# Kernel optimization log

Hardware: AMD Instinct MI355X
Metric: run time of the kernel (lower is better)

## Reference

```python
import jax, jax.numpy as jnp
import numpy as np

K = 10  # knn_graph default neighbors (self excluded)
NEG = 0.2  # LeakyReLU slope


def lrelu(x):
    return jnp.where(x > 0, x, NEG * x)


def conv1x1_1d(x, w):  # x: (B,Ci,N), w: (Co,Ci)
    return jnp.einsum('oi,bin->bon', w, x)


def conv1x1_2d(x, w):  # x: (B,Ci,N,k), w: (Co,Ci)
    return jnp.einsum('oi,bink->bonk', w, x)


def bn1(x, s, b):  # folded eval-mode BN, x: (B,C,N)
    return x * s[None, :, None] + b[None, :, None]


def bn2(x, s, b):  # x: (B,C,N,k)
    return x * s[None, :, None, None] + b[None, :, None, None]


def knn_graph(x, k=K):
    # x: (B, D, N) -> edge features (B, 2D, N, k)
    xt = jnp.transpose(x, (0, 2, 1))  # (B,N,D)
    sq = jnp.sum(xt * xt, axis=-1)  # (B,N)
    d2 = sq[:, :, None] + sq[:, None, :] - 2.0 * jnp.einsum('bnd,bmd->bnm', xt, xt)
    _, idx = jax.lax.top_k(-d2, k + 1)  # nearest k+1 incl. self
    idx = idx[:, :, 1:]  # drop self -> (B,N,k)
    B = xt.shape[0]
    feats = xt[jnp.arange(B)[:, None, None], idx]  # (B,N,k,D)
    center = xt[:, :, None, :]  # (B,N,1,D)
    edge = jnp.concatenate((feats - center, jnp.broadcast_to(center, feats.shape)), axis=-1)
    return jnp.transpose(edge, (0, 3, 1, 2))  # (B,2D,N,k)


def _make_params(key):
    ks = iter(jax.random.split(key, 32))
    def W(co, ci):
        return jax.random.normal(next(ks), (co, ci), jnp.float32) * (1.0 / np.sqrt(ci))
    def SB(c):
        return (jax.random.uniform(next(ks), (c,), jnp.float32, 0.5, 1.5),
                jax.random.normal(next(ks), (c,), jnp.float32) * 0.1)
    p = {}
    p['w1'] = W(64, 6);    p['s1'], p['b1'] = SB(64)
    p['w2'] = W(64, 64);   p['s2'], p['b2'] = SB(64)
    p['w3'] = W(64, 128);  p['s3'], p['b3'] = SB(64)
    p['w4'] = W(64, 64);   p['s4'], p['b4'] = SB(64)
    p['w5'] = W(64, 128);  p['s5'], p['b5'] = SB(64)
    p['w6'] = W(1024, 192); p['s6'], p['b6'] = SB(1024)
    p['w7'] = W(64, 16);   p['s7'], p['b7'] = SB(64)
    p['wp1'] = W(256, 1280); p['sp1'], p['bp1'] = SB(256)
    p['wp2'] = W(256, 256);  p['sp2'], p['bp2'] = SB(256)
    p['wp3'] = W(128, 256);  p['sp3'], p['bp3'] = SB(128)
    p['wp4'] = W(6, 128)
    return p


def setup_inputs() -> dict:
    key = jax.random.key(0)
    k0, k1, k2 = jax.random.split(key, 3)
    inp = {
        'points': jax.random.normal(k0, (8, 2048, 3), jnp.float32),
        'label': jax.random.uniform(k1, (8, 16), jnp.float32),
    }
    inp.update(_make_params(k2))
    return inp


def reference(points, label,
              w1, s1, b1, w2, s2, b2, w3, s3, b3, w4, s4, b4, w5, s5, b5,
              w6, s6, b6, w7, s7, b7,
              wp1, sp1, bp1, wp2, sp2, bp2, wp3, sp3, bp3, wp4):
    B, N, _ = points.shape
    x0 = jnp.transpose(points, (0, 2, 1))  # (B,3,N)

    e1 = knn_graph(x0)                                   # (B,6,N,k)
    h = lrelu(bn2(conv1x1_2d(e1, w1), s1, b1))
    out1 = jnp.max(lrelu(bn2(conv1x1_2d(h, w2), s2, b2)), axis=-1)  # (B,64,N)

    e2 = knn_graph(out1)                                 # (B,128,N,k)
    h = lrelu(bn2(conv1x1_2d(e2, w3), s3, b3))
    out2 = jnp.max(lrelu(bn2(conv1x1_2d(h, w4), s4, b4)), axis=-1)  # (B,64,N)

    e3 = knn_graph(out2)                                 # (B,128,N,k)
    out3 = jnp.max(lrelu(bn2(conv1x1_2d(e3, w5), s5, b5)), axis=-1)  # (B,64,N)

    comb = jnp.concatenate((out1, out2, out3), axis=1)   # (B,192,N)
    out4 = lrelu(bn1(conv1x1_1d(comb, w6), s6, b6))      # (B,1024,N)
    out4 = jnp.max(out4, axis=-1, keepdims=True)         # (B,1024,1)

    cat_vet = lrelu(bn1(conv1x1_1d(label[:, :, None], w7), s7, b7))  # (B,64,1)
    glob = jnp.broadcast_to(jnp.concatenate((out4, cat_vet), axis=1), (B, 1088, N))

    out = jnp.concatenate((out1, out2, out3, glob), axis=1)  # (B,1280,N)
    out = lrelu(bn1(conv1x1_1d(out, wp1), sp1, bp1))
    out = lrelu(bn1(conv1x1_1d(out, wp2), sp2, bp2))  # dropout = identity (eval)
    out = lrelu(bn1(conv1x1_1d(out, wp3), sp3, bp3))
    out = conv1x1_1d(out, wp4)                         # (B,6,N)
    return jnp.transpose(out, (0, 2, 1))               # (B,N,6)
```

## Files before the change

kernel.cpp:

```cpp
#include <hip/hip_runtime.h>
#include <float.h>

#define NEG 0.2f
constexpr int BATCH = 8;
constexpr int NPTS  = 2048;
constexpr int KNN   = 10;
constexpr int KP1   = 11;

__device__ __forceinline__ float lrelu(float x) { return x > 0.f ? x : NEG * x; }

__device__ __forceinline__ unsigned long long dkey(float d, int m) {
    unsigned u = __float_as_uint(d);
    u ^= (unsigned)((int)u >> 31) | 0x80000000u;
    return ((unsigned long long)u << 32) | (unsigned)m;
}

template<int D>
__global__ void sq_kernel(const float* __restrict__ xt, float* __restrict__ sq) {
    int i = blockIdx.x * 256 + threadIdx.x;
    if (i >= BATCH * NPTS) return;
    const float* p = xt + (size_t)i * D;
    float s = 0.f;
    #pragma unroll
    for (int d = 0; d < D; ++d) s += p[d] * p[d];
    sq[i] = s;
}

__global__ void sq64_kernel(const float* __restrict__ xt, float* __restrict__ sq) {
    int i = blockIdx.x * 256 + threadIdx.x;
    if (i >= BATCH * NPTS) return;
    const float4* p = (const float4*)(xt + (size_t)i * 64);
    float4 s4 = {0.f, 0.f, 0.f, 0.f};
    #pragma unroll
    for (int d = 0; d < 16; ++d) {
        float4 v = p[d];
        s4.x += v.x * v.x; s4.y += v.y * v.y; s4.z += v.z * v.z; s4.w += v.w * v.w;
    }
    sq[i] = (s4.x + s4.y) + (s4.z + s4.w);
}

__global__ __launch_bounds__(64) void knn3_kernel(const float* __restrict__ xt,
                                                  const float* __restrict__ sq,
                                                  int* __restrict__ idx_out) {
    const int bn = blockIdx.x;
    const int b  = bn >> 11;
    const int l  = threadIdx.x;

    const float qx = xt[(size_t)bn * 3 + 0];
    const float qy = xt[(size_t)bn * 3 + 1];
    const float qz = xt[(size_t)bn * 3 + 2];
    const float sqn = sq[bn];
    const float* xb  = xt + (size_t)b * NPTS * 3;
    const float* sqb_ = sq + (size_t)b * NPTS;

    unsigned long long lk[KP1];
    #pragma unroll
    for (int j = 0; j < KP1; ++j) lk[j] = ~0ULL;

    for (int m = l; m < NPTS; m += 64) {
        float dot = 0.f;
        dot += qx * xb[m * 3 + 0];
        dot += qy * xb[m * 3 + 1];
        dot += qz * xb[m * 3 + 2];
        float cd = sqn + sqb_[m] - 2.f * dot;
        unsigned long long key = dkey(cd, m);
        if (key < lk[KP1 - 1]) {
            #pragma unroll
            for (int j = 0; j < KP1; ++j) {
                bool better = key < lk[j];
                unsigned long long tk = lk[j];
                if (better) { lk[j] = key; key = tk; }
            }
        }
    }

    #pragma unroll
    for (int k = 0; k < KP1; ++k) {
        unsigned long long mk = lk[0];
        #pragma unroll
        for (int s = 32; s >= 1; s >>= 1) {
            unsigned long long o = __shfl_xor(mk, s, 64);
            mk = (o < mk) ? o : mk;
        }
        if (k >= 1 && l == k - 1)
            idx_out[(size_t)bn * KNN + (k - 1)] = (int)(unsigned)mk;
        if (lk[0] == mk) {
            #pragma unroll
            for (int j = 0; j < KP1 - 1; ++j) lk[j] = lk[j + 1];
            lk[KP1 - 1] = ~0ULL;
        }
    }
}

__global__ __launch_bounds__(256) void knn64_kernel(const float* __restrict__ xt,
                                                    const float* __restrict__ sq,
                                                    int* __restrict__ idx_out) {
    const int t  = threadIdx.x;
    const int qg = t >> 5;
    const int lc = t & 31;
    const int h  = qg & 1;
    const int w  = t >> 6;
    const int bn0 = blockIdx.x * 8;
    const int bn  = bn0 + qg;
    const int qA  = bn0 + 2 * w;
    const int qB  = qA + 1;
    const int b   = bn >> 11;
    const float* xb = xt + (size_t)b * NPTS * 64;

    __shared__ __align__(16) float4 tile4[2][32][16];

    float4 xqa[8], xqb[8];
    {
        const float4* pa = (const float4*)(xt + (size_t)qA * 64 + h * 32);
        const float4* pb = (const float4*)(xt + (size_t)qB * 64 + h * 32);
        #pragma unroll
        for (int i = 0; i < 8; ++i) { xqa[i] = pa[i]; xqb[i] = pb[i]; }
    }
    const float sqn = sq[bn];
    const float* sqb_ = sq + b * NPTS;

    unsigned long long lk[KP1];
    #pragma unroll
    for (int j = 0; j < KP1; ++j) lk[j] = ~0ULL;

    const int ci  = t >> 3;
    const int sub = t & 7;

    int ro[8];
    #pragma unroll
    for (int i = 0; i < 8; ++i) ro[i] = (h * 8 + i) ^ (lc & 15);
    const int wo0 = (2 * sub)     ^ (ci & 15);
    const int wo1 = (2 * sub + 1) ^ (ci & 15);

    const float4* rb0 = &tile4[0][lc][0];
    const float4* rb1 = &tile4[1][lc][0];
    float4*       wb0 = &tile4[0][ci][0];
    float4*       wb1 = &tile4[1][ci][0];

    const float4* src = (const float4*)(xb + (size_t)ci * 64 + sub * 8);

    {
        float4 u0 = src[0], u1 = src[1];
        wb0[wo0] = u0;
        wb0[wo1] = u1;
    }
    __syncthreads();
    src += 512;

    for (int t0 = 0; t0 < NPTS; t0 += 32) {
        float4 n0, n1;
        const bool more = (t0 + 32 < NPTS);
        if (more) { n0 = src[0]; n1 = src[1]; }

        float a0 = 0.f, a1 = 0.f, a2 = 0.f, a3 = 0.f;
        float c0 = 0.f, c1 = 0.f, c2 = 0.f, c3 = 0.f;
        #pragma unroll
        for (int i = 0; i < 8; ++i) {
            float4 v = rb0[ro[i]];
            a0 += xqa[i].x * v.x; a1 += xqa[i].y * v.y;
            a2 += xqa[i].z * v.z; a3 += xqa[i].w * v.w;
            c0 += xqb[i].x * v.x; c1 += xqb[i].y * v.y;
            c2 += xqb[i].z * v.z; c3 += xqb[i].w * v.w;
        }
        float pA = (a0 + a1) + (a2 + a3);
        float pB = (c0 + c1) + (c2 + c3);
        float oA = __shfl_xor(pA, 32, 64);
        float oB = __shfl_xor(pB, 32, 64);
        float dot = (h == 0) ? (pA + oA) : (oB + pB);

        const int m = t0 + lc;
        float cd = sqn + sqb_[m] - 2.f * dot;
        unsigned long long key = dkey(cd, m);
        if (key < lk[KP1 - 1]) {
            #pragma unroll
            for (int j = 0; j < KP1; ++j) {
                bool better = key < lk[j];
                unsigned long long tk = lk[j];
                if (better) { lk[j] = key; key = tk; }
            }
        }

        if (more) {
            wb1[wo0] = n0;
            wb1[wo1] = n1;
        }
        __syncthreads();
        { const float4* tr = rb0; rb0 = rb1; rb1 = tr; }
        { float4* tw = wb0; wb0 = wb1; wb1 = tw; }
        src += 512;
    }

    #pragma unroll
    for (int k = 0; k < KP1; ++k) {
        unsigned long long mk = lk[0];
        #pragma unroll
        for (int s = 16; s >= 1; s >>= 1) {
            unsigned long long o = __shfl_xor(mk, s, 32);
            mk = (o < mk) ? o : mk;
        }
        if (k >= 1 && lc == k - 1)
            idx_out[(size_t)bn * KNN + (k - 1)] = (int)(unsigned)mk;
        if (lk[0] == mk) {
            #pragma unroll
            for (int j = 0; j < KP1 - 1; ++j) lk[j] = lk[j + 1];
            lk[KP1 - 1] = ~0ULL;
        }
    }
}

__global__ __launch_bounds__(256) void edgeconv1_kernel(
    const float* __restrict__ pts, const int* __restrict__ idx,
    const float* __restrict__ w1, const float* __restrict__ s1, const float* __restrict__ b1,
    const float* __restrict__ w2, const float* __restrict__ s2, const float* __restrict__ b2,
    float* __restrict__ outt) {
    const int p0g = blockIdx.x * 8;
    const int b   = p0g >> 11;
    const int t   = threadIdx.x;
    const int p   = t >> 5;
    const int c32 = t & 31;
    const int pn  = p0g + p;
    const int c0 = c32, c1 = c32 + 32;

    __shared__ int   sidx[8][KNN];
    __shared__ float h1s[8][KNN][64];

    if (t < 8 * KNN) sidx[t / KNN][t % KNN] = idx[(size_t)(p0g + t / KNN) * KNN + (t % KNN)];
    __syncthreads();

    const float cx = pts[pn * 3 + 0], cy = pts[pn * 3 + 1], cz = pts[pn * 3 + 2];
    float w1r0[6], w1r1[6];
    #pragma unroll
    for (int i = 0; i < 6; ++i) { w1r0[i] = w1[c0 * 6 + i]; w1r1[i] = w1[c1 * 6 + i]; }
    const float s1c0 = s1[c0], b1c0 = b1[c0], s1c1 = s1[c1], b1c1 = b1[c1];

    #pragma unroll
    for (int k = 0; k < KNN; ++k) {
        const int m = sidx[p][k];
        const float* f = pts + ((size_t)b * NPTS + m) * 3;
        const float e0 = f[0] - cx, e1 = f[1] - cy, e2 = f[2] - cz;
        float a0 = w1r0[0] * e0 + w1r0[1] * e1 + w1r0[2] * e2
                 + w1r0[3] * cx + w1r0[4] * cy + w1r0[5] * cz;
        float a1 = w1r1[0] * e0 + w1r1[1] * e1 + w1r1[2] * e2
                 + w1r1[3] * cx + w1r1[4] * cy + w1r1[5] * cz;
        h1s[p][k][c0] = lrelu(a0 * s1c0 + b1c0);
        h1s[p][k][c1] = lrelu(a1 * s1c1 + b1c1);
    }
    __syncthreads();

    float a20[KNN], a21[KNN];
    #pragma unroll
    for (int k = 0; k < KNN; ++k) { a20[k] = 0.f; a21[k] = 0.f; }
    for (int j4 = 0; j4 < 16; ++j4) {
        float4 wv0 = *(const float4*)&w2[c0 * 64 + j4 * 4];
        float4 wv1 = *(const float4*)&w2[c1 * 64 + j4 * 4];
        #pragma unroll
        for (int k = 0; k < KNN; ++k) {
            float4 h4 = *(const float4*)&h1s[p][k][j4 * 4];
            a20[k] += wv0.x * h4.x + wv0.y * h4.y + wv0.z * h4.z + wv0.w * h4.w;
            a21[k] += wv1.x * h4.x + wv1.y * h4.y + wv1.z * h4.z + wv1.w * h4.w;
        }
    }
    const float s2c0 = s2[c0], b2c0 = b2[c0], s2c1 = s2[c1], b2c1 = b2[c1];
    float mx0 = -FLT_MAX, mx1 = -FLT_MAX;
    #pragma unroll
    for (int k = 0; k < KNN; ++k) {
        mx0 = fmaxf(mx0, lrelu(a20[k] * s2c0 + b2c0));
        mx1 = fmaxf(mx1, lrelu(a21[k] * s2c1 + b2c1));
    }
    outt[(size_t)pn * 64 + c0] = mx0;
    outt[(size_t)pn * 64 + c1] = mx1;
}

__global__ __launch_bounds__(256) void edgeconv2_kernel(
    const float* __restrict__ xin, const int* __restrict__ idx,
    const float* __restrict__ w3, const float* __restrict__ s3, const float* __restrict__ b3,
    const float* __restrict__ w4, const float* __restrict__ s4, const float* __restrict__ b4,
    float* __restrict__ outt) {
    const int p0g = blockIdx.x * 8;
    const int b   = p0g >> 11;
    const int t   = threadIdx.x;
    const int p   = t >> 5;
    const int c32 = t & 31;
    const int pn  = p0g + p;
    const int c0 = c32, c1 = c32 + 32;

    __shared__ int   sidx[8][KNN];
    __shared__ float cens[8][64];
    __shared__ float feas[8][KNN][64];
    __shared__ float h1s[8][KNN][64];

    if (t < 8 * KNN) sidx[t / KNN][t % KNN] = idx[(size_t)(p0g + t / KNN) * KNN + (t % KNN)];
    for (int i = t; i < 8 * 64; i += 256)
        cens[i >> 6][i & 63] = xin[((size_t)p0g + (i >> 6)) * 64 + (i & 63)];
    __syncthreads();
    for (int i = t; i < 8 * KNN * 64; i += 256) {
        int pp = i / (KNN * 64), r = i - pp * (KNN * 64);
        int k = r >> 6, c = r & 63;
        feas[pp][k][c] = xin[((size_t)b * NPTS + sidx[pp][k]) * 64 + c];
    }
    __syncthreads();

    float a0[KNN], a1[KNN];
    #pragma unroll
    for (int k = 0; k < KNN; ++k) { a0[k] = 0.f; a1[k] = 0.f; }
    float4 ab0 = {0.f, 0.f, 0.f, 0.f};
    float4 ab1 = {0.f, 0.f, 0.f, 0.f};
    for (int j4 = 0; j4 < 16; ++j4) {
        float4 wa0 = *(const float4*)&w3[c0 * 128 + j4 * 4];
        float4 wb0 = *(const float4*)&w3[c0 * 128 + 64 + j4 * 4];
        float4 wa1 = *(const float4*)&w3[c1 * 128 + j4 * 4];
        float4 wb1 = *(const float4*)&w3[c1 * 128 + 64 + j4 * 4];
        float4 c4 = *(const float4*)&cens[p][j4 * 4];
        ab0.x += (wb0.x - wa0.x) * c4.x; ab0.y += (wb0.y - wa0.y) * c4.y;
        ab0.z += (wb0.z - wa0.z) * c4.z; ab0.w += (wb0.w - wa0.w) * c4.w;
        ab1.x += (wb1.x - wa1.x) * c4.x; ab1.y += (wb1.y - wa1.y) * c4.y;
        ab1.z += (wb1.z - wa1.z) * c4.z; ab1.w += (wb1.w - wa1.w) * c4.w;
        #pragma unroll
        for (int k = 0; k < KNN; ++k) {
            float4 f4 = *(const float4*)&feas[p][k][j4 * 4];
            a0[k] += wa0.x * f4.x + wa0.y * f4.y + wa0.z * f4.z + wa0.w * f4.w;
            a1[k] += wa1.x * f4.x + wa1.y * f4.y + wa1.z * f4.z + wa1.w * f4.w;
        }
    }
    const float abase0 = (ab0.x + ab0.y) + (ab0.z + ab0.w);
    const float abase1 = (ab1.x + ab1.y) + (ab1.z + ab1.w);
    const float s3c0 = s3[c0], b3c0 = b3[c0], s3c1 = s3[c1], b3c1 = b3[c1];
    #pragma unroll
    for (int k = 0; k < KNN; ++k) {
        h1s[p][k][c0] = lrelu((a0[k] + abase0) * s3c0 + b3c0);
        h1s[p][k][c1] = lrelu((a1[k] + abase1) * s3c1 + b3c1);
    }
    __syncthreads();

    float a20[KNN], a21[KNN];
    #pragma unroll
    for (int k = 0; k < KNN; ++k) { a20[k] = 0.f; a21[k] = 0.f; }
    for (int j4 = 0; j4 < 16; ++j4) {
        float4 wv0 = *(const float4*)&w4[c0 * 64 + j4 * 4];
        float4 wv1 = *(const float4*)&w4[c1 * 64 + j4 * 4];
        #pragma unroll
        for (int k = 0; k < KNN; ++k) {
            float4 h4 = *(const float4*)&h1s[p][k][j4 * 4];
            a20[k] += wv0.x * h4.x + wv0.y * h4.y + wv0.z * h4.z + wv0.w * h4.w;
            a21[k] += wv1.x * h4.x + wv1.y * h4.y + wv1.z * h4.z + wv1.w * h4.w;
        }
    }
    const float s4c0 = s4[c0], b4c0 = b4[c0], s4c1 = s4[c1], b4c1 = b4[c1];
    float mx0 = -FLT_MAX, mx1 = -FLT_MAX;
    #pragma unroll
    for (int k = 0; k < KNN; ++k) {
        mx0 = fmaxf(mx0, lrelu(a20[k] * s4c0 + b4c0));
        mx1 = fmaxf(mx1, lrelu(a21[k] * s4c1 + b4c1));
    }
    outt[(size_t)pn * 64 + c0] = mx0;
    outt[(size_t)pn * 64 + c1] = mx1;
}

__global__ __launch_bounds__(256) void edgeconv3_kernel(
    const float* __restrict__ xin, const int* __restrict__ idx,
    const float* __restrict__ w5, const float* __restrict__ s5, const float* __restrict__ b5,
    float* __restrict__ outt) {
    const int p0g = blockIdx.x * 8;
    const int b   = p0g >> 11;
    const int t   = threadIdx.x;
    const int p   = t >> 5;
    const int c32 = t & 31;
    const int pn  = p0g + p;
    const int c0 = c32, c1 = c32 + 32;

    __shared__ int   sidx[8][KNN];
    __shared__ float cens[8][64];
    __shared__ float feas[8][KNN][64];

    if (t < 8 * KNN) sidx[t / KNN][t % KNN] = idx[(size_t)(p0g + t / KNN) * KNN + (t % KNN)];
    for (int i = t; i < 8 * 64; i += 256)
        cens[i >> 6][i & 63] = xin[((size_t)p0g + (i >> 6)) * 64 + (i & 63)];
    __syncthreads();
    for (int i = t; i < 8 * KNN * 64; i += 256) {
        int pp = i / (KNN * 64), r = i - pp * (KNN * 64);
        int k = r >> 6, c = r & 63;
        feas[pp][k][c] = xin[((size_t)b * NPTS + sidx[pp][k]) * 64 + c];
    }
    __syncthreads();

    float a0[KNN], a1[KNN];
    #pragma unroll
    for (int k = 0; k < KNN; ++k) { a0[k] = 0.f; a1[k] = 0.f; }
    float4 ab0 = {0.f, 0.f, 0.f, 0.f};
    float4 ab1 = {0.f, 0.f, 0.f, 0.f};
    for (int j4 = 0; j4 < 16; ++j4) {
        float4 wa0 = *(const float4*)&w5[c0 * 128 + j4 * 4];
        float4 wb0 = *(const float4*)&w5[c0 * 128 + 64 + j4 * 4];
        float4 wa1 = *(const float4*)&w5[c1 * 128 + j4 * 4];
        float4 wb1 = *(const float4*)&w5[c1 * 128 + 64 + j4 * 4];
        float4 c4 = *(const float4*)&cens[p][j4 * 4];
        ab0.x += (wb0.x - wa0.x) * c4.x; ab0.y += (wb0.y - wa0.y) * c4.y;
        ab0.z += (wb0.z - wa0.z) * c4.z; ab0.w += (wb0.w - wa0.w) * c4.w;
        ab1.x += (wb1.x - wa1.x) * c4.x; ab1.y += (wb1.y - wa1.y) * c4.y;
        ab1.z += (wb1.z - wa1.z) * c4.z; ab1.w += (wb1.w - wa1.w) * c4.w;
        #pragma unroll
        for (int k = 0; k < KNN; ++k) {
            float4 f4 = *(const float4*)&feas[p][k][j4 * 4];
            a0[k] += wa0.x * f4.x + wa0.y * f4.y + wa0.z * f4.z + wa0.w * f4.w;
            a1[k] += wa1.x * f4.x + wa1.y * f4.y + wa1.z * f4.z + wa1.w * f4.w;
        }
    }
    const float abase0 = (ab0.x + ab0.y) + (ab0.z + ab0.w);
    const float abase1 = (ab1.x + ab1.y) + (ab1.z + ab1.w);
    const float s5c0 = s5[c0], b5c0 = b5[c0], s5c1 = s5[c1], b5c1 = b5[c1];
    float mx0 = -FLT_MAX, mx1 = -FLT_MAX;
    #pragma unroll
    for (int k = 0; k < KNN; ++k) {
        mx0 = fmaxf(mx0, lrelu((a0[k] + abase0) * s5c0 + b5c0));
        mx1 = fmaxf(mx1, lrelu((a1[k] + abase1) * s5c1 + b5c1));
    }
    outt[(size_t)pn * 64 + c0] = mx0;
    outt[(size_t)pn * 64 + c1] = mx1;
}

__global__ __launch_bounds__(64) void catvet_kernel(
    const float* __restrict__ label,
    const float* __restrict__ w7, const float* __restrict__ s7, const float* __restrict__ b7,
    float* __restrict__ catv) {
    const int b = blockIdx.x, c = threadIdx.x;
    float a = 0.f;
    #pragma unroll
    for (int i = 0; i < 16; ++i) a += w7[c * 16 + i] * label[b * 16 + i];
    catv[b * 64 + c] = lrelu(a * s7[c] + b7[c]);
}

__global__ void w6t_kernel(const float* __restrict__ w6, float* __restrict__ w6t) {
    int i = blockIdx.x * 256 + threadIdx.x;
    if (i >= 192 * 1024) return;
    int k = i >> 10, c = i & 1023;
    w6t[i] = w6[c * 192 + k];
}

constexpr int OPTS = 32;
__global__ __launch_bounds__(256) void out4max_kernel(
    const float* __restrict__ out1t, const float* __restrict__ out2t, const float* __restrict__ out3t,
    const float* __restrict__ w6t, float* __restrict__ partial) {
    const int blk = blockIdx.x;
    const int b   = blk >> 6;
    const int nt  = blk & 63;
    const int t   = threadIdx.x;

    __shared__ float xs[192 * OPTS];
    for (int idx = t; idx < 192 * OPTS; idx += 256) {
        int p = idx / 192, r = idx - p * 192;
        const size_t gp = (size_t)b * NPTS + nt * OPTS + p;
        float val;
        if (r < 64)       val = out1t[gp * 64 + r];
        else if (r < 128) val = out2t[gp * 64 + (r - 64)];
        else              val = out3t[gp * 64 + (r - 128)];
        xs[r * OPTS + p] = val;
    }
    __syncthreads();

    float mx0 = -FLT_MAX, mx1 = -FLT_MAX, mx2 = -FLT_MAX, mx3 = -FLT_MAX;
    #pragma unroll
    for (int pg = 0; pg < OPTS / 16; ++pg) {
        float acc0[16], acc1[16], acc2[16], acc3[16];
        #pragma unroll
        for (int p = 0; p < 16; ++p) { acc0[p] = 0.f; acc1[p] = 0.f; acc2[p] = 0.f; acc3[p] = 0.f; }
        #pragma unroll 2
        for (int k = 0; k < 192; ++k) {
            float4 wv = *(const float4*)&w6t[(size_t)k * 1024 + t * 4];
            const float4* xr4 = (const float4*)&xs[k * OPTS + pg * 16];
            #pragma unroll
            for (int p4 = 0; p4 < 4; ++p4) {
                float4 xv = xr4[p4];
                acc0[p4 * 4 + 0] += wv.x * xv.x; acc0[p4 * 4 + 1] += wv.x * xv.y;
                acc0[p4 * 4 + 2] += wv.x * xv.z; acc0[p4 * 4 + 3] += wv.x * xv.w;
                acc1[p4 * 4 + 0] += wv.y * xv.x; acc1[p4 * 4 + 1] += wv.y * xv.y;
                acc1[p4 * 4 + 2] += wv.y * xv.z; acc1[p4 * 4 + 3] += wv.y * xv.w;
                acc2[p4 * 4 + 0] += wv.z * xv.x; acc2[p4 * 4 + 1] += wv.z * xv.y;
                acc2[p4 * 4 + 2] += wv.z * xv.z; acc2[p4 * 4 + 3] += wv.z * xv.w;
                acc3[p4 * 4 + 0] += wv.w * xv.x; acc3[p4 * 4 + 1] += wv.w * xv.y;
                acc3[p4 * 4 + 2] += wv.w * xv.z; acc3[p4 * 4 + 3] += wv.w * xv.w;
            }
        }
        #pragma unroll
        for (int p = 0; p < 16; ++p) {
            mx0 = fmaxf(mx0, acc0[p]); mx1 = fmaxf(mx1, acc1[p]);
            mx2 = fmaxf(mx2, acc2[p]); mx3 = fmaxf(mx3, acc3[p]);
        }
    }
    float4 o = {mx0, mx1, mx2, mx3};
    *(float4*)&partial[(size_t)blk * 1024 + t * 4] = o;
}

__global__ __launch_bounds__(256) void out4reduce_kernel(
    const float* __restrict__ partial,
    const float* __restrict__ s6, const float* __restrict__ b6,
    float* __restrict__ out4m) {
    const int i = blockIdx.x * 256 + threadIdx.x;
    const int b = i >> 10, c = i & 1023;
    float m = -FLT_MAX;
    for (int nt = 0; nt < 64; ++nt)
        m = fmaxf(m, partial[((size_t)b * 64 + nt) * 1024 + c]);
    out4m[i] = lrelu(m * s6[c] + b6[c]);
}

__global__ __launch_bounds__(256) void gbias_kernel(
    const float* __restrict__ out4m, const float* __restrict__ catv,
    const float* __restrict__ wp1, float* __restrict__ g) {
    const int b = blockIdx.x, t = threadIdx.x;
    __shared__ float v[1088];
    for (int i = t; i < 1088; i += 256)
        v[i] = (i < 1024) ? out4m[(size_t)b * 1024 + i] : catv[(size_t)b * 64 + (i - 1024)];
    __syncthreads();
    const float* w = wp1 + (size_t)t * 1280 + 192;
    float4 s4 = {0.f, 0.f, 0.f, 0.f};
    for (int i = 0; i < 272; ++i) {
        float4 wv = *(const float4*)&w[i * 4];
        float4 vv = *(const float4*)&v[i * 4];
        s4.x += wv.x * vv.x; s4.y += wv.y * vv.y; s4.z += wv.z * vv.z; s4.w += wv.w * vv.w;
    }
    g[(size_t)b * 256 + t] = (s4.x + s4.y) + (s4.z + s4.w);
}

constexpr int HP = 16;
constexpr int KC = 16;

__global__ __launch_bounds__(256) void head_kernel(
    const float* __restrict__ out1t, const float* __restrict__ out2t, const float* __restrict__ out3t,
    const float* __restrict__ g,
    const float* __restrict__ wp1, const float* __restrict__ sp1, const float* __restrict__ bp1,
    const float* __restrict__ wp2, const float* __restrict__ sp2, const float* __restrict__ bp2,
    const float* __restrict__ wp3, const float* __restrict__ sp3, const float* __restrict__ bp3,
    const float* __restrict__ wp4, float* __restrict__ out) {
    const int p0 = blockIdx.x * HP;
    const int b  = p0 >> 11;
    const int t  = threadIdx.x;

    __shared__ float smA[4096];
    __shared__ float smB[4096];
    __shared__ float smW[KC * 256];

    for (int e = t; e < 192 * HP; e += 256) {
        int p = e / 192, k = e - p * 192;
        float val;
        if (k < 64)       val = out1t[((size_t)(p0 + p)) * 64 + k];
        else if (k < 128) val = out2t[((size_t)(p0 + p)) * 64 + (k - 64)];
        else              val = out3t[((size_t)(p0 + p)) * 64 + (k - 128)];
        smA[k * HP + p] = val;
    }

    const int og = t & 31;
    const int pg = t >> 5;

    float acc[2][8];
    #pragma unroll
    for (int i = 0; i < 8; ++i) {
        float gv = g[(size_t)b * 256 + og * 8 + i];
        acc[0][i] = gv; acc[1][i] = gv;
    }
    for (int kc = 0; kc < 192 / KC; ++kc) {
        __syncthreads();
        #pragma unroll
        for (int it = 0; it < KC; ++it)
            smW[it * 256 + t] = wp1[(size_t)t * 1280 + kc * KC + it];
        __syncthreads();
        #pragma unroll 4
        for (int kk = 0; kk < KC; ++kk) {
            int k = kc * KC + kk;
            float2 xv = *(const float2*)&smA[k * HP + pg * 2];
            float4 w0 = *(const float4*)&smW[kk * 256 + og * 8];
            float4 w1v = *(const float4*)&smW[kk * 256 + og * 8 + 4];
            float wv[8] = {w0.x, w0.y, w0.z, w0.w, w1v.x, w1v.y, w1v.z, w1v.w};
            #pragma unroll
            for (int i = 0; i < 8; ++i) {
                acc[0][i] += xv.x * wv[i];
                acc[1][i] += xv.y * wv[i];
            }
        }
    }
    #pragma unroll
    for (int i = 0; i < 8; ++i) {
        int o = og * 8 + i;
        float sc = sp1[o], bc = bp1[o];
        smB[o * HP + pg * 2 + 0] = lrelu(acc[0][i] * sc + bc);
        smB[o * HP + pg * 2 + 1] = lrelu(acc[1][i] * sc + bc);
    }

    float acc2[2][8];
    #pragma unroll
    for (int i = 0; i < 8; ++i) { acc2[0][i] = 0.f; acc2[1][i] = 0.f; }
    for (int kc = 0; kc < 256 / KC; ++kc) {
        __syncthreads();
        #pragma unroll
        for (int it = 0; it < KC; ++it)
            smW[it * 256 + t] = wp2[(size_t)t * 256 + kc * KC + it];
        __syncthreads();
        #pragma unroll 4
        for (int kk = 0; kk < KC; ++kk) {
            int k = kc * KC + kk;
            float2 xv = *(const float2*)&smB[k * HP + pg * 2];
            float4 w0 = *(const float4*)&smW[kk * 256 + og * 8];
            float4 w1v = *(const float4*)&smW[kk * 256 + og * 8 + 4];
            float wv[8] = {w0.x, w0.y, w0.z, w0.w, w1v.x, w1v.y, w1v.z, w1v.w};
            #pragma unroll
            for (int i = 0; i < 8; ++i) {
                acc2[0][i] += xv.x * wv[i];
                acc2[1][i] += xv.y * wv[i];
            }
        }
    }
    __syncthreads();
    #pragma unroll
    for (int i = 0; i < 8; ++i) {
        int o = og * 8 + i;
        float sc = sp2[o], bc = bp2[o];
        smA[o * HP + pg * 2 + 0] = lrelu(acc2[0][i] * sc + bc);
        smA[o * HP + pg * 2 + 1] = lrelu(acc2[1][i] * sc + bc);
    }

    const int og3 = t & 15;
    const int p3  = t >> 4;
    float acc3[8];
    #pragma unroll
    for (int i = 0; i < 8; ++i) acc3[i] = 0.f;
    for (int kc = 0; kc < 256 / KC; ++kc) {
        __syncthreads();
        for (int e = t; e < KC * 128; e += 256) {
            int kk = e >> 7, o = e & 127;
            smW[kk * 128 + o] = wp3[(size_t)o * 256 + kc * KC + kk];
        }
        __syncthreads();
        #pragma unroll 4
        for (int kk = 0; kk < KC; ++kk) {
            int k = kc * KC + kk;
            float xv = smA[k * HP + p3];
            float4 w0 = *(const float4*)&smW[kk * 128 + og3 * 8];
            float4 w1v = *(const float4*)&smW[kk * 128 + og3 * 8 + 4];
            float wv[8] = {w0.x, w0.y, w0.z, w0.w, w1v.x, w1v.y, w1v.z, w1v.w};
            #pragma unroll
            for (int i = 0; i < 8; ++i) acc3[i] += xv * wv[i];
        }
    }
    __syncthreads();
    #pragma unroll
    for (int i = 0; i < 8; ++i) {
        int o = og3 * 8 + i;
        float sc = sp3[o], bc = bp3[o];
        smB[o * HP + p3] = lrelu(acc3[i] * sc + bc);
    }
    __syncthreads();

    if (t < HP * 6) {
        int p = t / 6, o = t - p * 6;
        float4 s4 = {0.f, 0.f, 0.f, 0.f};
        for (int k4 = 0; k4 < 32; ++k4) {
            float4 wv = *(const float4*)&wp4[o * 128 + k4 * 4];
            s4.x += wv.x * smB[(k4 * 4 + 0) * HP + p];
            s4.y += wv.y * smB[(k4 * 4 + 1) * HP + p];
            s4.z += wv.z * smB[(k4 * 4 + 2) * HP + p];
            s4.w += wv.w * smB[(k4 * 4 + 3) * HP + p];
        }
        out[((size_t)(p0 + p)) * 6 + o] = (s4.x + s4.y) + (s4.z + s4.w);
    }
}

extern "C" void kernel_launch(void* const* d_in, const int* in_sizes, int n_in,
                              void* d_out, int out_size, void* d_ws, size_t ws_size,
                              hipStream_t stream) {
    const float* points = (const float*)d_in[0];
    const float* label  = (const float*)d_in[1];
    const float* w1  = (const float*)d_in[2];
    const float* s1  = (const float*)d_in[3];
    const float* b1  = (const float*)d_in[4];
    const float* w2  = (const float*)d_in[5];
    const float* s2  = (const float*)d_in[6];
    const float* b2  = (const float*)d_in[7];
    const float* w3  = (const float*)d_in[8];
    const float* s3  = (const float*)d_in[9];
    const float* b3  = (const float*)d_in[10];
    const float* w4  = (const float*)d_in[11];
    const float* s4  = (const float*)d_in[12];
    const float* b4  = (const float*)d_in[13];
    const float* w5  = (const float*)d_in[14];
    const float* s5  = (const float*)d_in[15];
    const float* b5  = (const float*)d_in[16];
    const float* w6  = (const float*)d_in[17];
    const float* s6  = (const float*)d_in[18];
    const float* b6  = (const float*)d_in[19];
    const float* w7  = (const float*)d_in[20];
    const float* s7  = (const float*)d_in[21];
    const float* b7  = (const float*)d_in[22];
    const float* wp1 = (const float*)d_in[23];
    const float* sp1 = (const float*)d_in[24];
    const float* bp1 = (const float*)d_in[25];
    const float* wp2 = (const float*)d_in[26];
    const float* sp2 = (const float*)d_in[27];
    const float* bp2 = (const float*)d_in[28];
    const float* wp3 = (const float*)d_in[29];
    const float* sp3 = (const float*)d_in[30];
    const float* bp3 = (const float*)d_in[31];
    const float* wp4 = (const float*)d_in[32];

    float* ws = (float*)d_ws;
    size_t off = 0;
    auto alloc = [&](size_t nf) { float* p = ws + off; off += nf; return p; };
    float* out1t = alloc((size_t)BATCH * NPTS * 64);
    float* out2t = alloc((size_t)BATCH * NPTS * 64);
    float* out3t = alloc((size_t)BATCH * NPTS * 64);
    float* sqb   = alloc((size_t)BATCH * NPTS);
    float* out4m = alloc((size_t)BATCH * 1024);
    float* catv  = alloc((size_t)BATCH * 64);
    float* gb    = alloc((size_t)BATCH * 256);
    float* w6t   = alloc((size_t)192 * 1024);
    float* part  = alloc((size_t)512 * 1024);
    int* idx1 = (int*)alloc((size_t)BATCH * NPTS * KNN);
    int* idx2 = (int*)alloc((size_t)BATCH * NPTS * KNN);
    int* idx3 = (int*)alloc((size_t)BATCH * NPTS * KNN);

    const int BN = BATCH * NPTS;
    const int sqBlocks = (BN + 255) / 256;

    sq_kernel<3><<<sqBlocks, 256, 0, stream>>>(points, sqb);
    knn3_kernel<<<BN, 64, 0, stream>>>(points, sqb, idx1);
    edgeconv1_kernel<<<BN / 8, 256, 0, stream>>>(points, idx1, w1, s1, b1, w2, s2, b2, out1t);

    sq64_kernel<<<sqBlocks, 256, 0, stream>>>(out1t, sqb);
    knn64_kernel<<<BN / 8, 256, 0, stream>>>(out1t, sqb, idx2);
    edgeconv2_kernel<<<BN / 8, 256, 0, stream>>>(out1t, idx2, w3, s3, b3, w4, s4, b4, out2t);

    sq64_kernel<<<sqBlocks, 256, 0, stream>>>(out2t, sqb);
    knn64_kernel<<<BN / 8, 256, 0, stream>>>(out2t, sqb, idx3);
    edgeconv3_kernel<<<BN / 8, 256, 0, stream>>>(out2t, idx3, w5, s5, b5, out3t);

    catvet_kernel<<<BATCH, 64, 0, stream>>>(label, w7, s7, b7, catv);
    w6t_kernel<<<(192 * 1024 + 255) / 256, 256, 0, stream>>>(w6, w6t);
    out4max_kernel<<<512, 256, 0, stream>>>(out1t, out2t, out3t, w6t, part);
    out4reduce_kernel<<<BATCH * 1024 / 256, 256, 0, stream>>>(part, s6, b6, out4m);
    gbias_kernel<<<BATCH, 256, 0, stream>>>(out4m, catv, wp1, gb);

    head_kernel<<<BN / HP, 256, 0, stream>>>(out1t, out2t, out3t, gb,
                                             wp1, sp1, bp1, wp2, sp2, bp2, wp3, sp3, bp3,
                                             wp4, (float*)d_out);
}
```

Before: 1.099 ms.

## Pre-transpose head weights and double points per head block

Adds a kernel that transposes wp1/wp2/wp3 into k-major layout so the head kernel can stage weight chunks into shared memory with coalesced float4 loads, replacing strided per-thread row reads. The head kernel now processes 32 points per block instead of 16, and each thread accumulates 4 (or 2) points per output group. This halves how often weights are reloaded per point and raises arithmetic intensity. In exchange it uses more registers and twice the shared memory per block, which may lower occupancy, and it adds an extra transpose launch. w6t_kernel is also moved earlier in the launch order.

```diff
diff --git a/kernel.cpp b/kernel.cpp
--- a/kernel.cpp
+++ b/kernel.cpp
@@ -436,6 +436,29 @@
     w6t[i] = w6[c * 192 + k];
 }
 
+__global__ void wpt_kernel(const float* __restrict__ wp1, const float* __restrict__ wp2,
+                           const float* __restrict__ wp3,
+                           float* __restrict__ wp1t, float* __restrict__ wp2t,
+                           float* __restrict__ wp3t) {
+    int i = blockIdx.x * 256 + threadIdx.x;
+    if (i < 192 * 256) {
+        int k = i >> 8, o = i & 255;
+        wp1t[i] = wp1[(size_t)o * 1280 + k];
+        return;
+    }
+    i -= 192 * 256;
+    if (i < 256 * 256) {
+        int k = i >> 8, o = i & 255;
+        wp2t[i] = wp2[(size_t)o * 256 + k];
+        return;
+    }
+    i -= 256 * 256;
+    if (i < 256 * 128) {
+        int k = i >> 7, o = i & 127;
+        wp3t[i] = wp3[(size_t)o * 256 + k];
+    }
+}
+
 constexpr int OPTS = 32;
 __global__ __launch_bounds__(256) void out4max_kernel(
     const float* __restrict__ out1t, const float* __restrict__ out2t, const float* __restrict__ out3t,
@@ -520,23 +543,23 @@
     g[(size_t)b * 256 + t] = (s4.x + s4.y) + (s4.z + s4.w);
 }
 
-constexpr int HP = 16;
+constexpr int HP = 32;
 constexpr int KC = 16;
 
 __global__ __launch_bounds__(256) void head_kernel(
     const float* __restrict__ out1t, const float* __restrict__ out2t, const float* __restrict__ out3t,
     const float* __restrict__ g,
-    const float* __restrict__ wp1, const float* __restrict__ sp1, const float* __restrict__ bp1,
-    const float* __restrict__ wp2, const float* __restrict__ sp2, const float* __restrict__ bp2,
-    const float* __restrict__ wp3, const float* __restrict__ sp3, const float* __restrict__ bp3,
+    const float* __restrict__ wp1t, const float* __restrict__ sp1, const float* __restrict__ bp1,
+    const float* __restrict__ wp2t, const float* __restrict__ sp2, const float* __restrict__ bp2,
+    const float* __restrict__ wp3t, const float* __restrict__ sp3, const float* __restrict__ bp3,
     const float* __restrict__ wp4, float* __restrict__ out) {
     const int p0 = blockIdx.x * HP;
     const int b  = p0 >> 11;
     const int t  = threadIdx.x;
 
-    __shared__ float smA[4096];
-    __shared__ float smB[4096];
-    __shared__ float smW[KC * 256];
+    __shared__ float smA[8192];
+    __shared__ float smB[8192];
+    __shared__ __align__(16) float smW[KC * 256];
 
     for (int e = t; e < 192 * HP; e += 256) {
         int p = e / 192, k = e - p * 192;
@@ -550,22 +573,25 @@
     const int og = t & 31;
     const int pg = t >> 5;
 
-    float acc[2][8];
+    float acc[4][8];
     #pragma unroll
     for (int i = 0; i < 8; ++i) {
         float gv = g[(size_t)b * 256 + og * 8 + i];
-        acc[0][i] = gv; acc[1][i] = gv;
+        acc[0][i] = gv; acc[1][i] = gv; acc[2][i] = gv; acc[3][i] = gv;
     }
     for (int kc = 0; kc < 192 / KC; ++kc) {
         __syncthreads();
-        #pragma unroll
-        for (int it = 0; it < KC; ++it)
-            smW[it * 256 + t] = wp1[(size_t)t * 1280 + kc * KC + it];
+        {
+            const float4* wsrc = (const float4*)(wp1t + (size_t)kc * KC * 256);
+            float4* wdst = (float4*)smW;
+            #pragma unroll
+            for (int r = 0; r < 4; ++r) wdst[t + r * 256] = wsrc[t + r * 256];
+        }
         __syncthreads();
         #pragma unroll 4
         for (int kk = 0; kk < KC; ++kk) {
             int k = kc * KC + kk;
-            float2 xv = *(const float2*)&smA[k * HP + pg * 2];
+            float4 xv = *(const float4*)&smA[k * HP + pg * 4];
             float4 w0 = *(const float4*)&smW[kk * 256 + og * 8];
             float4 w1v = *(const float4*)&smW[kk * 256 + og * 8 + 4];
             float wv[8] = {w0.x, w0.y, w0.z, w0.w, w1v.x, w1v.y, w1v.z, w1v.w};
@@ -573,30 +599,38 @@
             for (int i = 0; i < 8; ++i) {
                 acc[0][i] += xv.x * wv[i];
                 acc[1][i] += xv.y * wv[i];
+                acc[2][i] += xv.z * wv[i];
+                acc[3][i] += xv.w * wv[i];
             }
         }
     }
+    __syncthreads();
     #pragma unroll
     for (int i = 0; i < 8; ++i) {
         int o = og * 8 + i;
         float sc = sp1[o], bc = bp1[o];
-        smB[o * HP + pg * 2 + 0] = lrelu(acc[0][i] * sc + bc);
-        smB[o * HP + pg * 2 + 1] = lrelu(acc[1][i] * sc + bc);
-    }
-
-    float acc2[2][8];
-    #pragma unroll
-    for (int i = 0; i < 8; ++i) { acc2[0][i] = 0.f; acc2[1][i] = 0.f; }
+        smB[o * HP + pg * 4 + 0] = lrelu(acc[0][i] * sc + bc);
+        smB[o * HP + pg * 4 + 1] = lrelu(acc[1][i] * sc + bc);
+        smB[o * HP + pg * 4 + 2] = lrelu(acc[2][i] * sc + bc);
+        smB[o * HP + pg * 4 + 3] = lrelu(acc[3][i] * sc + bc);
+    }
+
+    float acc2[4][8];
+    #pragma unroll
+    for (int i = 0; i < 8; ++i) { acc2[0][i] = 0.f; acc2[1][i] = 0.f; acc2[2][i] = 0.f; acc2[3][i] = 0.f; }
     for (int kc = 0; kc < 256 / KC; ++kc) {
         __syncthreads();
-        #pragma unroll
-        for (int it = 0; it < KC; ++it)
-            smW[it * 256 + t] = wp2[(size_t)t * 256 + kc * KC + it];
+        {
+            const float4* wsrc = (const float4*)(wp2t + (size_t)kc * KC * 256);
+            float4* wdst = (float4*)smW;
+            #pragma unroll
+            for (int r = 0; r < 4; ++r) wdst[t + r * 256] = wsrc[t + r * 256];
+        }
         __syncthreads();
         #pragma unroll 4
         for (int kk = 0; kk < KC; ++kk) {
             int k = kc * KC + kk;
-            float2 xv = *(const float2*)&smB[k * HP + pg * 2];
+            float4 xv = *(const float4*)&smB[k * HP + pg * 4];
             float4 w0 = *(const float4*)&smW[kk * 256 + og * 8];
             float4 w1v = *(const float4*)&smW[kk * 256 + og * 8 + 4];
             float wv[8] = {w0.x, w0.y, w0.z, w0.w, w1v.x, w1v.y, w1v.z, w1v.w};
@@ -604,6 +638,8 @@
             for (int i = 0; i < 8; ++i) {
                 acc2[0][i] += xv.x * wv[i];
                 acc2[1][i] += xv.y * wv[i];
+                acc2[2][i] += xv.z * wv[i];
+                acc2[3][i] += xv.w * wv[i];
             }
         }
     }
@@ -612,31 +648,39 @@
     for (int i = 0; i < 8; ++i) {
         int o = og * 8 + i;
         float sc = sp2[o], bc = bp2[o];
-        smA[o * HP + pg * 2 + 0] = lrelu(acc2[0][i] * sc + bc);
-        smA[o * HP + pg * 2 + 1] = lrelu(acc2[1][i] * sc + bc);
+        smA[o * HP + pg * 4 + 0] = lrelu(acc2[0][i] * sc + bc);
+        smA[o * HP + pg * 4 + 1] = lrelu(acc2[1][i] * sc + bc);
+        smA[o * HP + pg * 4 + 2] = lrelu(acc2[2][i] * sc + bc);
+        smA[o * HP + pg * 4 + 3] = lrelu(acc2[3][i] * sc + bc);
     }
 
     const int og3 = t & 15;
-    const int p3  = t >> 4;
-    float acc3[8];
-    #pragma unroll
-    for (int i = 0; i < 8; ++i) acc3[i] = 0.f;
+    const int pg3 = t >> 4;
+    float acc3[2][8];
+    #pragma unroll
+    for (int i = 0; i < 8; ++i) { acc3[0][i] = 0.f; acc3[1][i] = 0.f; }
     for (int kc = 0; kc < 256 / KC; ++kc) {
         __syncthreads();
-        for (int e = t; e < KC * 128; e += 256) {
-            int kk = e >> 7, o = e & 127;
-            smW[kk * 128 + o] = wp3[(size_t)o * 256 + kc * KC + kk];
+        {
+            const float4* wsrc = (const float4*)(wp3t + (size_t)kc * KC * 128);
+            float4* wdst = (float4*)smW;
+            #pragma unroll
+            for (int r = 0; r < 2; ++r) wdst[t + r * 256] = wsrc[t + r * 256];
         }
         __syncthreads();
         #pragma unroll 4
         for (int kk = 0; kk < KC; ++kk) {
             int k = kc * KC + kk;
-            float xv = smA[k * HP + p3];
+            float xv0 = smA[k * HP + pg3];
+            float xv1 = smA[k * HP + 16 + pg3];
             float4 w0 = *(const float4*)&smW[kk * 128 + og3 * 8];
             float4 w1v = *(const float4*)&smW[kk * 128 + og3 * 8 + 4];
             float wv[8] = {w0.x, w0.y, w0.z, w0.w, w1v.x, w1v.y, w1v.z, w1v.w};
             #pragma unroll
-            for (int i = 0; i < 8; ++i) acc3[i] += xv * wv[i];
+            for (int i = 0; i < 8; ++i) {
+                acc3[0][i] += xv0 * wv[i];
+                acc3[1][i] += xv1 * wv[i];
+            }
         }
     }
     __syncthreads();
@@ -644,7 +688,8 @@
     for (int i = 0; i < 8; ++i) {
         int o = og3 * 8 + i;
         float sc = sp3[o], bc = bp3[o];
-        smB[o * HP + p3] = lrelu(acc3[i] * sc + bc);
+        smB[o * HP + pg3]      = lrelu(acc3[0][i] * sc + bc);
+        smB[o * HP + 16 + pg3] = lrelu(acc3[1][i] * sc + bc);
     }
     __syncthreads();
 
@@ -711,6 +756,9 @@
     float* gb    = alloc((size_t)BATCH * 256);
     float* w6t   = alloc((size_t)192 * 1024);
     float* part  = alloc((size_t)512 * 1024);
+    float* wp1t  = alloc((size_t)192 * 256);
+    float* wp2t  = alloc((size_t)256 * 256);
+    float* wp3t  = alloc((size_t)256 * 128);
     int* idx1 = (int*)alloc((size_t)BATCH * NPTS * KNN);
     int* idx2 = (int*)alloc((size_t)BATCH * NPTS * KNN);
     int* idx3 = (int*)alloc((size_t)BATCH * NPTS * KNN);
@@ -718,6 +766,9 @@
     const int BN = BATCH * NPTS;
     const int sqBlocks = (BN + 255) / 256;
 
+    w6t_kernel<<<(192 * 1024 + 255) / 256, 256, 0, stream>>>(w6, w6t);
+    wpt_kernel<<<(147456 + 255) / 256, 256, 0, stream>>>(wp1, wp2, wp3, wp1t, wp2t, wp3t);
+
     sq_kernel<3><<<sqBlocks, 256, 0, stream>>>(points, sqb);
     knn3_kernel<<<BN, 64, 0, stream>>>(points, sqb, idx1);
     edgeconv1_kernel<<<BN / 8, 256, 0, stream>>>(points, idx1, w1, s1, b1, w2, s2, b2, out1t);
@@ -731,12 +782,11 @@
     edgeconv3_kernel<<<BN / 8, 256, 0, stream>>>(out2t, idx3, w5, s5, b5, out3t);
 
     catvet_kernel<<<BATCH, 64, 0, stream>>>(label, w7, s7, b7, catv);
-    w6t_kernel<<<(192 * 1024 + 255) / 256, 256, 0, stream>>>(w6, w6t);
     out4max_kernel<<<512, 256, 0, stream>>>(out1t, out2t, out3t, w6t, part);
     out4reduce_kernel<<<BATCH * 1024 / 256, 256, 0, stream>>>(part, s6, b6, out4m);
     gbias_kernel<<<BATCH, 256, 0, stream>>>(out4m, catv, wp1, gb);
 
     head_kernel<<<BN / HP, 256, 0, stream>>>(out1t, out2t, out3t, gb,
-                                             wp1, sp1, bp1, wp2, sp2, bp2, wp3, sp3, bp3,
+                                             wp1t, sp1, bp1, wp2t, sp2, bp2, wp3t, sp3, bp3,
                                              wp4, (float*)d_out);
 }
```

New measurement: 974.4 us (median of 2 runs). 11.4% less time.
